# Kernel optimization log

Measured on AMD Instinct MI355X. Metric: run time of the kernel, lower is better.

## Reference

```python
import jax, jax.numpy as jnp
import numpy as np

K = 7          # kernel_size
PAD = K // 2
NAZ, NEL = 12, 5
HID = 64
IC = 2         # input_channels == num_instruments
OC = 2         # output_channels (stereo)
EPS = 1e-5


def conv1d_same(x, w, b):
    # x: (N, Cin, T), w: (Cout, Cin, K) -> (N, Cout, T); cross-correlation like torch
    y = jax.lax.conv_general_dilated(x, w, (1,), 'SAME',
                                     dimension_numbers=('NCH', 'OIH', 'NCH'))
    return y + b[None, :, None]


def batchnorm(x, g, bt):
    # training-mode BatchNorm1d: biased batch stats over (N, T)
    mean = x.mean(axis=(0, 2), keepdims=True)
    var = x.var(axis=(0, 2), keepdims=True)
    return (x - mean) * jax.lax.rsqrt(var + EPS) * g[None, :, None] + bt[None, :, None]


def lrelu(x):
    return jnp.where(x >= 0, x, 0.2 * x)


def setup_inputs() -> dict:
    key = jax.random.key(0)
    ks = jax.random.split(key, 16)
    d = {}
    d['x'] = jax.random.normal(ks[0], (8, IC, 131072), dtype=jnp.float32)
    # spatial_param_net
    d['W1'] = jax.random.normal(ks[1], (HID, IC, K), dtype=jnp.float32) * 0.1
    d['b1'] = jnp.zeros((HID,), jnp.float32)
    d['g1'] = jnp.ones((HID,), jnp.float32)
    d['be1'] = jnp.zeros((HID,), jnp.float32)
    d['W2'] = jax.random.normal(ks[2], (2 * HID, HID, K), dtype=jnp.float32) * 0.05
    d['b2'] = jnp.zeros((2 * HID,), jnp.float32)
    d['g2'] = jnp.ones((2 * HID,), jnp.float32)
    d['be2'] = jnp.zeros((2 * HID,), jnp.float32)
    d['W3'] = jax.random.normal(ks[3], (IC * 3, 2 * HID, K), dtype=jnp.float32) * 0.05
    d['b3'] = jnp.zeros((IC * 3,), jnp.float32)
    # HRTF table: (num_azimuth*num_elevation, output_channels, K)
    d['hrtf'] = jax.random.normal(ks[4], (NAZ * NEL, OC, K), dtype=jnp.float32)
    # binaural_renderer (first conv in-channels = input_channels = 2)
    d['RW1'] = jax.random.normal(ks[5], (HID, IC, K), dtype=jnp.float32) * 0.1
    d['rb1'] = jnp.zeros((HID,), jnp.float32)
    d['rg1'] = jnp.ones((HID,), jnp.float32)
    d['rbe1'] = jnp.zeros((HID,), jnp.float32)
    d['RW2'] = jax.random.normal(ks[6], (2 * HID, HID, K), dtype=jnp.float32) * 0.05
    d['rb2'] = jnp.zeros((2 * HID,), jnp.float32)
    d['rg2'] = jnp.ones((2 * HID,), jnp.float32)
    d['rbe2'] = jnp.zeros((2 * HID,), jnp.float32)
    d['RW3'] = jax.random.normal(ks[7], (OC, 2 * HID, K), dtype=jnp.float32) * 0.05
    d['rb3'] = jnp.zeros((OC,), jnp.float32)
    return d


def reference(x, W1, b1, g1, be1, W2, b2, g2, be2, W3, b3, hrtf,
              RW1, rb1, rg1, rbe1, RW2, rb2, rg2, rbe2, RW3, rb3):
    B, I, T = x.shape
    # spatial parameter network
    h = lrelu(batchnorm(conv1d_same(x, W1, b1), g1, be1))
    h = lrelu(batchnorm(conv1d_same(h, W2, b2), g2, be2))
    sp = jnp.tanh(conv1d_same(h, W3, b3)).reshape(B, I, 3, T)
    # only t=0 of azimuth/elevation/distance is used (matches torch loop)
    az = (sp[:, :, 0, 0] + 1.0) * 0.5 * (NAZ - 1)
    el = (sp[:, :, 1, 0] + 1.0) * 0.5 * (NEL - 1)
    dist = (sp[:, :, 2, 0] + 1.0) * 0.5 * 0.9 + 0.1      # (B, I)
    az_i = jnp.clip(az.astype(jnp.int32), 0, NAZ - 1)
    el_i = jnp.clip(el.astype(jnp.int32), 0, NEL - 1)
    idx = el_i * NAZ + az_i                               # (B, I)
    wg = hrtf[idx]                                        # (B, I, OC, K) gathered filters
    # per-(b,i) conv1d with its gathered HRTF filter, scale by distance, sum over instruments
    xp = jnp.pad(x, ((0, 0), (0, 0), (PAD, PAD)))
    windows = jnp.stack([xp[:, :, k:k + T] for k in range(K)], axis=2)  # (B, I, K, T)
    summed = jnp.einsum('bikt,bick,bi->bct', windows, wg, dist)          # (B, OC, T)
    # binaural renderer
    h = lrelu(batchnorm(conv1d_same(summed, RW1, rb1), rg1, rbe1))
    h = lrelu(batchnorm(conv1d_same(h, RW2, rb2), rg2, rbe2))
    return jnp.tanh(conv1d_same(h, RW3, rb3))
```

## Files before the change

kernel.cpp:

```cpp
#include <hip/hip_runtime.h>
#include <hip/hip_fp16.h>
#include <cstddef>


#define TLEN 131072
#define NB 8
#define NICH 2
#define NHID 64
#define NH2 128
#define EPSV 1e-5f
#define CNTF 1048576.0f
#define FT 120
#define FGRID 1093
#define XCH 1024
#define NCH 128
#define XGRID 1024
#define PREPB 472

typedef _Float16 f16x8 __attribute__((ext_vector_type(8)));
typedef float f32x4 __attribute__((ext_vector_type(4)));

__device__ __forceinline__ float lrelu(float v) { return fmaxf(v, 0.2f * v); }
__device__ __forceinline__ unsigned short h16(float v) {
  return __half_as_ushort(__float2half(v));
}
__device__ __forceinline__ float fh16(unsigned short u) {
  return __half2float(__ushort_as_half(u));
}
__device__ __forceinline__ float ftanh(float x) {
  float e = __expf(2.f * x);
  return 1.f - 2.f / (e + 1.f);
}

__device__ __forceinline__ void prep_body(
    int e,
    const float* __restrict__ W2c, const float* __restrict__ RW2c,
    const float* __restrict__ RW3c,
    const float* __restrict__ W1c, const float* __restrict__ RW1c,
    unsigned short* __restrict__ w2sp, unsigned short* __restrict__ w2re,
    unsigned short* __restrict__ w3g,
    unsigned short* __restrict__ w1sp, unsigned short* __restrict__ w1re)
{
  if (e < 114688) {
    int e2 = (e >= 57344) ? e - 57344 : e;
    int frag = e2 >> 9, within = e2 & 511;
    int c = frag >> 3, mt = frag & 7;
    int mn = within >> 5, kk = within & 31;
    int o = mt * 16 + mn;
    int tap = c >> 1, ch = (c & 1) * 32 + kk;
    const float* src = (e >= 57344) ? RW2c : W2c;
    unsigned short* dst = (e >= 57344) ? w2re : w2sp;
    dst[e2] = h16(src[(o * 64 + ch) * 7 + tap]);
  } else if (e < 116736) {
    int e2 = e - 114688;
    int c = e2 >> 9, within = e2 & 511;
    int m = within >> 5, kk = within & 31;
    int ch = c * 32 + kk;
    w3g[e2] = (m < 14) ? h16(RW3c[((m / 7) * 128 + ch) * 7 + (m % 7)])
                       : (unsigned short)0;
  } else if (e < 120832) {
    int e2 = e - 116736;
    int which = (e2 >= 2048);
    int e3 = e2 & 2047;
    int m = e3 >> 9, w = e3 & 511;
    int mn = w >> 5, K = w & 31;
    int i = K >> 4, kk = K & 15;
    const float* src = which ? RW1c : W1c;
    unsigned short* dst = which ? w1re : w1sp;
    dst[e3] = (kk < 7) ? h16(src[(m * 16 + mn) * 14 + i * 7 + kk])
                       : (unsigned short)0;
  }
}

__device__ __forceinline__ void xcorr_reduce_tail(
    float (&acc)[30], float (*redx)[30], float* __restrict__ partials)
{
  #pragma unroll
  for (int q = 0; q < 30; ++q)
    #pragma unroll
    for (int m = 1; m <= 8; m <<= 1)
      acc[q] += __shfl_xor(acc[q], m, 64);
  const int lane = threadIdx.x & 63, wv = threadIdx.x >> 6;
  if ((lane & 15) == 0) {
    int row = wv * 4 + (lane >> 4);
    #pragma unroll
    for (int q = 0; q < 30; ++q) redx[row][q] = acc[q];
  }
  __syncthreads();
  if (threadIdx.x < 30) {
    float s = 0.f;
    #pragma unroll
    for (int r = 0; r < 16; ++r) s += redx[r][threadIdx.x];
    partials[blockIdx.x * 30 + threadIdx.x] = s;
  }
}

__global__ __launch_bounds__(256) void xcorr_prep(
    const float* __restrict__ z, float* __restrict__ partials,
    const float* __restrict__ W2c, const float* __restrict__ RW2c,
    const float* __restrict__ RW3c,
    const float* __restrict__ W1c, const float* __restrict__ RW1c,
    unsigned short* __restrict__ w2sp, unsigned short* __restrict__ w2re,
    unsigned short* __restrict__ w3g,
    unsigned short* __restrict__ w1sp, unsigned short* __restrict__ w1re)
{
  if (blockIdx.x >= XGRID) {
    int e = (blockIdx.x - XGRID) * 256 + threadIdx.x;
    prep_body(e, W2c, RW2c, RW3c, W1c, RW1c, w2sp, w2re, w3g, w1sp, w1re);
    return;
  }
  const int b = blockIdx.x >> 7;
  const int t0 = (blockIdx.x & (NCH - 1)) * XCH;
  __shared__ float zs[2][XCH + 8];
  __shared__ float redx[16][30];
  #pragma unroll
  for (int i = 0; i < 2; ++i) {
    const float* zp = &z[(size_t)(b * 2 + i) * TLEN + t0];
    *(float4*)&zs[i][threadIdx.x * 4] = *(const float4*)&zp[threadIdx.x * 4];
    if (threadIdx.x < 7) {
      int tg = t0 + XCH + threadIdx.x;
      zs[i][XCH + threadIdx.x] =
          (tg < TLEN) ? z[(size_t)(b * 2 + i) * TLEN + tg] : 0.f;
    }
    if (threadIdx.x == 7) zs[i][XCH + 7] = 0.f;
  }
  __syncthreads();

  float acc[30];
  #pragma unroll
  for (int q = 0; q < 30; ++q) acc[q] = 0.f;
  const int tb = threadIdx.x * 4;
  #pragma unroll
  for (int tt = 0; tt < 4; ++tt) {
    int j = tb + tt;
    float z0 = zs[0][j], z1 = zs[1][j];
    acc[28] += z0; acc[29] += z1;
    #pragma unroll
    for (int d = 0; d < 7; ++d) {
      float a0 = zs[0][j + d], a1 = zs[1][j + d];
      acc[d]      += z0 * a0;
      acc[7 + d]  += z0 * a1;
      acc[14 + d] += z1 * a0;
      acc[21 + d] += z1 * a1;
    }
  }
  xcorr_reduce_tail(acc, redx, partials);
}

__global__ __launch_bounds__(256) void reduce30(
    const float* __restrict__ partials, int nblocks, float* __restrict__ R)
{
  const int q = blockIdx.x;
  float s = 0.f;
  for (int j = threadIdx.x; j < nblocks; j += 256)
    s += partials[j * 30 + q];
  #pragma unroll
  for (int m = 1; m <= 32; m <<= 1) s += __shfl_xor(s, m, 64);
  __shared__ float rs[4];
  if ((threadIdx.x & 63) == 0) rs[threadIdx.x >> 6] = s;
  __syncthreads();
  if (threadIdx.x == 0) R[q] = rs[0] + rs[1] + rs[2] + rs[3];
}

__global__ __launch_bounds__(256) void assemble_coef1(
    const float* __restrict__ Rg,
    const float* __restrict__ W1c, const float* __restrict__ b1c,
    const float* __restrict__ g, const float* __restrict__ be,
    float* __restrict__ coef)
{
  __shared__ float R[30];
  __shared__ float w1s[64 * 14];
  for (int e = threadIdx.x; e < 64 * 14; e += 256) w1s[e] = W1c[e];
  if (threadIdx.x < 30) R[threadIdx.x] = Rg[threadIdx.x];
  __syncthreads();
  if (threadIdx.x < 64) {
    int o = threadIdx.x;
    const float* w = &w1s[o * 14];
    float b1v = b1c[o];
    float sy = 0.f;
    #pragma unroll
    for (int i = 0; i < 2; ++i)
      #pragma unroll
      for (int k = 0; k < 7; ++k) sy += w[i * 7 + k] * R[28 + i];
    float syy = 0.f;
    #pragma unroll
    for (int i = 0; i < 2; ++i)
      #pragma unroll
      for (int k = 0; k < 7; ++k) {
        float wv = w[i * 7 + k];
        #pragma unroll
        for (int i2 = 0; i2 < 2; ++i2)
          #pragma unroll
          for (int k2 = 0; k2 < 7; ++k2) {
            int d = k2 - k;
            float r = (d >= 0) ? R[i * 14 + i2 * 7 + d]
                               : R[i2 * 14 + i * 7 - d];
            syy += wv * w[i2 * 7 + k2] * r;
          }
      }
    float S1 = CNTF * b1v + sy;
    float S2 = 2.f * b1v * S1 - CNTF * b1v * b1v + syy;
    float mean = S1 / CNTF;
    float var = S2 / CNTF - mean * mean;
    float a = g[o] * rsqrtf(var + EPSV);
    coef[o] = a;
    coef[64 + o] = be[o] - mean * a;
  }
}

__global__ __launch_bounds__(256) void reduce_coef(
    const float* __restrict__ partials, int nblocks, int C,
    const float* __restrict__ bso,
    const float* __restrict__ g, const float* __restrict__ be,
    float* __restrict__ coef)
{
  const int c = blockIdx.x;
  float s = 0.f, ss = 0.f;
  for (int j = threadIdx.x; j < nblocks; j += 256) {
    s  += partials[j * 2 * C + c];
    ss += partials[j * 2 * C + C + c];
  }
  #pragma unroll
  for (int off = 32; off >= 1; off >>= 1) {
    s  += __shfl_down(s, off, 64);
    ss += __shfl_down(ss, off, 64);
  }
  __shared__ float rs[4], rss[4];
  const int lane = threadIdx.x & 63, wv = threadIdx.x >> 6;
  if (lane == 0) { rs[wv] = s; rss[wv] = ss; }
  __syncthreads();
  if (threadIdx.x == 0) {
    float st  = rs[0] + rs[1] + rs[2] + rs[3];
    float sst = rss[0] + rss[1] + rss[2] + rss[3];
    float mean = st / CNTF;
    float var  = sst / CNTF - mean * mean;
    float a = g[c] * rsqrtf(var + EPSV);
    float d = be[c] - mean * a;
    coef[c] = a;
    coef[C + c] = d;
    coef[2 * C + c] = d + a * bso[c];
  }
}

__device__ __forceinline__ void stage_x(
    int t0, int xoff, const float* __restrict__ xin, int b, float* xs)
{
  for (int e = threadIdx.x; e < 2 * 168; e += 256) {
    int i = e / 168, j = e % 168;
    int tg = t0 - xoff + j;
    xs[e] = (tg >= 0 && tg < TLEN) ? xin[(b * NICH + i) * TLEN + tg] : 0.f;
  }
}

template<int HOF>
__device__ __forceinline__ void h1_mfma(
    int t0, const float* xs, unsigned short* xw,
    const unsigned short* __restrict__ w1f,
    const float* __restrict__ coef1, const float* __restrict__ b1c,
    unsigned short* h1f)
{
  for (int e = threadIdx.x; e < 144 * 2; e += 256) {
    int n = e >> 1, i = e & 1;
    const float* xp = &xs[i * 168 + n];
    unsigned short hv[7];
    #pragma unroll
    for (int kk = 0; kk < 7; ++kk) hv[kk] = h16(xp[kk]);
    *(uint4*)(xw + n * 32 + i * 16) = make_uint4(
        hv[0] | ((unsigned)hv[1] << 16), hv[2] | ((unsigned)hv[3] << 16),
        hv[4] | ((unsigned)hv[5] << 16), (unsigned)hv[6]);
    *(uint4*)(xw + n * 32 + i * 16 + 8) = make_uint4(0, 0, 0, 0);
  }
  __syncthreads();

  const int lane = threadIdx.x & 63;
  const int wv = threadIdx.x >> 6;
  const int mn = lane & 15, quad = lane >> 4;
  f16x8 A1 = *(const f16x8*)(w1f + wv * 512 + mn * 32 + quad * 8);
  f32x4 acc1[9];
  #pragma unroll
  for (int nt = 0; nt < 9; ++nt) {
    f32x4 z = {0.f, 0.f, 0.f, 0.f};
    acc1[nt] = z;
  }
  #pragma unroll
  for (int nt = 0; nt < 9; ++nt) {
    f16x8 bb = *(const f16x8*)(xw + (nt * 16 + mn) * 32 + quad * 8);
    acc1[nt] = __builtin_amdgcn_mfma_f32_16x16x32_f16(A1, bb, acc1[nt], 0, 0, 0);
  }
  const int ch0 = wv * 16 + quad * 4;
  float a1v[4], dd[4];
  #pragma unroll
  for (int r = 0; r < 4; ++r) {
    a1v[r] = coef1[ch0 + r];
    dd[r]  = coef1[64 + ch0 + r] + a1v[r] * b1c[ch0 + r];
  }
  #pragma unroll
  for (int nt = 0; nt < 9; ++nt) {
    int n = nt * 16 + mn;
    int t = t0 - HOF + n;
    bool ok = (t >= 0) && (t < TLEN);
    unsigned us[4];
    #pragma unroll
    for (int r = 0; r < 4; ++r) {
      float v = lrelu(a1v[r] * acc1[nt][r] + dd[r]);
      us[r] = h16(ok ? v : 0.f);
    }
    *(uint2*)(h1f + n * 72 + ch0) =
        make_uint2(us[0] | (us[1] << 16), us[2] | (us[3] << 16));
  }
}

template<int SAVE>
__global__ __launch_bounds__(256, 4) void conv2_stats_mfma(
    const float* __restrict__ xin,
    const unsigned short* __restrict__ w1f, const float* __restrict__ b1c,
    const float* __restrict__ coef1,
    const unsigned short* __restrict__ w2f,
    const float* __restrict__ b2c,
    float* __restrict__ partials,
    unsigned short* __restrict__ h1out)
{
  const int b  = blockIdx.x >> 10;
  const int t0 = (blockIdx.x & 1023) * 128;

  __shared__ __align__(16) char smem[31296];
  unsigned short* h1f = (unsigned short*)smem;
  float* xs = (float*)(smem + 20736);
  unsigned short* xw = (unsigned short*)(smem + 22080);
  float* redS = (float*)smem;
  float* redSS= (float*)(smem + 8704);

  stage_x(t0, 6, xin, b, xs);
  __syncthreads();
  h1_mfma<3>(t0, xs, xw, w1f, coef1, b1c, h1f);
  __syncthreads();

  if (SAVE == 1) {
    for (int e = threadIdx.x; e < 1024; e += 256) {
      int row = e >> 3, c8 = (e & 7) * 8;
      *(uint4*)(h1out + ((size_t)(b * TLEN + t0 + row) * 64 + c8)) =
          *(const uint4*)(h1f + (row + 3) * 72 + c8);
    }
  }

  const int lane = threadIdx.x & 63;
  const int wv = threadIdx.x >> 6;
  const int mn = lane & 15, quad = lane >> 4;

  f32x4 acc[2][8];
  #pragma unroll
  for (int mt = 0; mt < 2; ++mt)
    #pragma unroll
    for (int nt = 0; nt < 8; ++nt) {
      f32x4 z = {0.f, 0.f, 0.f, 0.f};
      acc[mt][nt] = z;
    }

  f16x8 ca[2], na[2];
  auto loadA = [&](int c, f16x8 (&A)[2]) {
    #pragma unroll
    for (int mt = 0; mt < 2; ++mt)
      A[mt] = *(const f16x8*)(w2f + (c * 8 + wv * 2 + mt) * 512 + mn * 32 + quad * 8);
  };
  loadA(0, ca);
  #pragma unroll
  for (int c = 0; c < 14; ++c) {
    if (c < 13) loadA(c + 1, na);
    const int tap = c >> 1;
    const int ch0 = (c & 1) * 32 + quad * 8;
    #pragma unroll
    for (int nt = 0; nt < 8; ++nt) {
      f16x8 bb = *(const f16x8*)(h1f + (nt * 16 + mn + tap) * 72 + ch0);
      acc[0][nt] = __builtin_amdgcn_mfma_f32_16x16x32_f16(ca[0], bb, acc[0][nt], 0, 0, 0);
      acc[1][nt] = __builtin_amdgcn_mfma_f32_16x16x32_f16(ca[1], bb, acc[1][nt], 0, 0, 0);
    }
    ca[0] = na[0]; ca[1] = na[1];
  }
  __syncthreads();

  #pragma unroll
  for (int mt = 0; mt < 2; ++mt)
    #pragma unroll
    for (int r = 0; r < 4; ++r) {
      int o = (wv * 2 + mt) * 16 + quad * 4 + r;
      float bo = b2c[o];
      float s = 0.f, ss = 0.f;
      #pragma unroll
      for (int nt = 0; nt < 8; ++nt) {
        float v = acc[mt][nt][r] + bo;
        s += v; ss += v * v;
      }
      redS[o * 17 + mn] = s;
      redSS[o * 17 + mn] = ss;
    }
  __syncthreads();
  {
    int o = threadIdx.x & 127;
    const float* src = (threadIdx.x < 128) ? redS : redSS;
    float s = 0.f;
    #pragma unroll
    for (int j = 0; j < 16; ++j) s += src[o * 17 + j];
    partials[blockIdx.x * 256 + threadIdx.x] = s;
  }
}

__global__ __launch_bounds__(256) void finalize_spatial(
    const float* __restrict__ x,
    const float* __restrict__ W1c, const float* __restrict__ b1c,
    const float* __restrict__ coef1,
    const float* __restrict__ W2c, const float* __restrict__ b2c,
    const float* __restrict__ coef2,
    const float* __restrict__ W3c, const float* __restrict__ b3c,
    const float* __restrict__ hrtf, float* __restrict__ wgbuf)
{
  const int bb = blockIdx.x;
  __shared__ float xl[2 * 16];
  __shared__ float h1l[64 * 10];
  __shared__ float h2l[NH2 * 4];
  __shared__ float sp[6];
  const int tid = threadIdx.x;
  if (tid < 32) {
    int i = tid >> 4, j = tid & 15;
    int t = j - 6;
    xl[tid] = (t >= 0) ? x[(bb * 2 + i) * TLEN + t] : 0.f;
  }
  __syncthreads();
  if (tid < 64) {
    int ch = tid;
    float a1 = coef1[ch], d1 = coef1[64 + ch], bo = b1c[ch];
    for (int tt = 0; tt < 10; ++tt) {
      float acc = bo;
      #pragma unroll
      for (int i2 = 0; i2 < 2; ++i2)
        #pragma unroll
        for (int k = 0; k < 7; ++k)
          acc += xl[i2 * 16 + tt + k] * W1c[ch * 14 + i2 * 7 + k];
      float v = lrelu(a1 * acc + d1);
      h1l[ch * 10 + tt] = (tt >= 3) ? v : 0.f;
    }
  }
  __syncthreads();
  if (tid < NH2) {
    int o = tid;
    float a2 = coef2[o], d2 = coef2[NH2 + o], bo = b2c[o];
    float acc[4] = {bo, bo, bo, bo};
    for (int i = 0; i < 64; ++i)
      #pragma unroll
      for (int k = 0; k < 7; ++k) {
        float w = W2c[(o * 64 + i) * 7 + k];
        #pragma unroll
        for (int t = 0; t < 4; ++t)
          acc[t] += h1l[i * 10 + t + k] * w;
      }
    #pragma unroll
    for (int t = 0; t < 4; ++t)
      h2l[o * 4 + t] = lrelu(a2 * acc[t] + d2);
  }
  __syncthreads();
  if (tid < 6) {
    int c3 = tid;
    float acc = b3c[c3];
    for (int c = 0; c < NH2; ++c)
      #pragma unroll
      for (int k = 3; k < 7; ++k)
        acc += h2l[c * 4 + (k - 3)] * W3c[(c3 * NH2 + c) * 7 + k];
    sp[c3] = tanhf(acc);
  }
  __syncthreads();
  if (tid < 2) {
    int i = tid;
    float az = (sp[i * 3 + 0] + 1.f) * 0.5f * 11.f;
    float el = (sp[i * 3 + 1] + 1.f) * 0.5f * 4.f;
    float dist = (sp[i * 3 + 2] + 1.f) * 0.5f * 0.9f + 0.1f;
    int azi = min(max((int)az, 0), 11);
    int eli = min(max((int)el, 0), 4);
    int idx = eli * 12 + azi;
    for (int e = 0; e < 14; ++e)
      wgbuf[(bb * 2 + i) * 14 + e] = hrtf[idx * 14 + e] * dist;
  }
}

__global__ __launch_bounds__(256) void mix_xcorr(
    const float* __restrict__ x, const float* __restrict__ wgbuf,
    float* __restrict__ summed, float* __restrict__ partials)
{
  const int b = blockIdx.x >> 7;
  const int t0 = (blockIdx.x & (NCH - 1)) * XCH;
  const int tid = threadIdx.x;
  __shared__ float xs2[2][XCH + 20];
  __shared__ float zs[2][XCH + 8];
  __shared__ float redx[16][30];

  float wv[2][2][7];
  #pragma unroll
  for (int i = 0; i < 2; ++i)
    #pragma unroll
    for (int c = 0; c < 2; ++c)
      #pragma unroll
      for (int k = 0; k < 7; ++k)
        wv[i][c][k] = wgbuf[(b * 2 + i) * 14 + c * 7 + k];

  const bool interior = (t0 >= 8) && (t0 + XCH + 12 <= TLEN);
  if (interior) {
    #pragma unroll
    for (int i = 0; i < 2; ++i) {
      const float* xp = &x[(size_t)(b * 2 + i) * TLEN + t0 - 8];
      *(float4*)&xs2[i][tid * 4] = *(const float4*)&xp[tid * 4];
      if (tid < 5)
        *(float4*)&xs2[i][XCH + tid * 4] = *(const float4*)&xp[XCH + tid * 4];
    }
  } else {
    for (int e = tid; e < 2 * (XCH + 20); e += 256) {
      int i = e / (XCH + 20), j = e % (XCH + 20);
      int tg = t0 - 8 + j;
      xs2[i][j] = (tg >= 0 && tg < TLEN) ? x[(size_t)(b * 2 + i) * TLEN + tg]
                                         : 0.f;
    }
  }
  __syncthreads();

  const int tb = tid * 4;
  {
    float xl[2][10];
    #pragma unroll
    for (int i = 0; i < 2; ++i)
      #pragma unroll
      for (int j = 0; j < 10; ++j) xl[i][j] = xs2[i][tb + 5 + j];
    float acc[2][4] = {{0.f, 0.f, 0.f, 0.f}, {0.f, 0.f, 0.f, 0.f}};
    #pragma unroll
    for (int i = 0; i < 2; ++i)
      #pragma unroll
      for (int c = 0; c < 2; ++c)
        #pragma unroll
        for (int k = 0; k < 7; ++k)
          #pragma unroll
          for (int tt = 0; tt < 4; ++tt)
            acc[c][tt] += xl[i][tt + k] * wv[i][c][k];
    #pragma unroll
    for (int c = 0; c < 2; ++c) {
      *(float4*)&zs[c][tb] =
          make_float4(acc[c][0], acc[c][1], acc[c][2], acc[c][3]);
      *reinterpret_cast<float4*>(&summed[(size_t)(b * 2 + c) * TLEN + t0 + tb]) =
          make_float4(acc[c][0], acc[c][1], acc[c][2], acc[c][3]);
    }
  }
  if (tid < 7) {
    int t = t0 + XCH + tid;
    float s0 = 0.f, s1 = 0.f;
    if (t < TLEN) {
      #pragma unroll
      for (int i = 0; i < 2; ++i)
        #pragma unroll
        for (int k = 0; k < 7; ++k) {
          float xv = xs2[i][XCH + tid + 5 + k];
          s0 += xv * wv[i][0][k];
          s1 += xv * wv[i][1][k];
        }
    }
    zs[0][XCH + tid] = s0;
    zs[1][XCH + tid] = s1;
  }
  if (tid == 7) { zs[0][XCH + 7] = 0.f; zs[1][XCH + 7] = 0.f; }
  __syncthreads();

  float acc[30];
  #pragma unroll
  for (int q = 0; q < 30; ++q) acc[q] = 0.f;
  #pragma unroll
  for (int tt = 0; tt < 4; ++tt) {
    int j = tb + tt;
    float z0 = zs[0][j], z1 = zs[1][j];
    acc[28] += z0; acc[29] += z1;
    #pragma unroll
    for (int d = 0; d < 7; ++d) {
      float a0 = zs[0][j + d], a1 = zs[1][j + d];
      acc[d]      += z0 * a0;
      acc[7 + d]  += z0 * a1;
      acc[14 + d] += z1 * a0;
      acc[21 + d] += z1 * a1;
    }
  }
  xcorr_reduce_tail(acc, redx, partials);
}

__device__ __forceinline__ void final_tail(
    int b, int t0, f32x4 (&acc)[2][8],
    const float* __restrict__ coef2,
    const unsigned short* __restrict__ w3g, const float* __restrict__ rb3c,
    unsigned short* h2t, unsigned short* dq, float* __restrict__ out)
{
  const int lane = threadIdx.x & 63;
  const int wv = threadIdx.x >> 6;
  const int mn = lane & 15, quad = lane >> 4;

  float a2v[2][4], dd2[2][4];
  #pragma unroll
  for (int mt = 0; mt < 2; ++mt)
    #pragma unroll
    for (int r = 0; r < 4; ++r) {
      int o = (wv * 2 + mt) * 16 + quad * 4 + r;
      a2v[mt][r] = coef2[o];
      dd2[mt][r] = coef2[2 * NH2 + o];
    }
  __syncthreads();

  #pragma unroll
  for (int nt = 0; nt < 8; ++nt) {
    int jp = nt * 16 + mn;
    int t = t0 - 3 + jp;
    bool ok = (t >= 0) && (t < TLEN);
    #pragma unroll
    for (int mt = 0; mt < 2; ++mt) {
      int obase = (wv * 2 + mt) * 16 + quad * 4;
      unsigned us[4];
      #pragma unroll
      for (int r = 0; r < 4; ++r) {
        float v = lrelu(a2v[mt][r] * acc[mt][nt][r] + dd2[mt][r]);
        us[r] = h16(ok ? v : 0.f);
      }
      *(uint2*)(h2t + jp * 136 + obase) =
          make_uint2(us[0] | (us[1] << 16), us[2] | (us[3] << 16));
    }
  }
  __syncthreads();

  const int nt0 = wv * 2;
  f32x4 acc3[2];
  #pragma unroll
  for (int i = 0; i < 2; ++i) {
    f32x4 z = {0.f, 0.f, 0.f, 0.f};
    acc3[i] = z;
  }
  #pragma unroll
  for (int c = 0; c < 4; ++c) {
    f16x8 A3 = *(const f16x8*)(w3g + c * 512 + mn * 32 + quad * 8);
    #pragma unroll
    for (int i = 0; i < 2; ++i) {
      f16x8 bb = *(const f16x8*)(h2t + ((nt0 + i) * 16 + mn) * 136 + c * 32 + quad * 8);
      acc3[i] = __builtin_amdgcn_mfma_f32_16x16x32_f16(A3, bb, acc3[i], 0, 0, 0);
    }
  }
  #pragma unroll
  for (int i = 0; i < 2; ++i) {
    int n = (nt0 + i) * 16 + mn;
    unsigned us[4];
    #pragma unroll
    for (int r = 0; r < 4; ++r) us[r] = h16(acc3[i][r]);
    *(uint2*)(dq + n * 20 + quad * 4) =
        make_uint2(us[0] | (us[1] << 16), us[2] | (us[3] << 16));
  }
  __syncthreads();

  {
    int tid = threadIdx.x;
    if (tid < 240) {
      int oc = (tid >= FT) ? 1 : 0;
      int u = tid - oc * FT;
      float s = rb3c[oc];
      #pragma unroll
      for (int tap = 0; tap < 7; ++tap)
        s += fh16(dq[(u + tap) * 20 + oc * 7 + tap]);
      int t = t0 + u;
      if (t < TLEN) out[(b * 2 + oc) * TLEN + t] = ftanh(s);
    }
  }
}

__device__ __forceinline__ void conv2_loop(
    const unsigned short* h1f, const unsigned short* __restrict__ w2f,
    f32x4 (&acc)[2][8])
{
  const int lane = threadIdx.x & 63;
  const int wv = threadIdx.x >> 6;
  const int mn = lane & 15, quad = lane >> 4;
  #pragma unroll
  for (int mt = 0; mt < 2; ++mt)
    #pragma unroll
    for (int nt = 0; nt < 8; ++nt) {
      f32x4 z = {0.f, 0.f, 0.f, 0.f};
      acc[mt][nt] = z;
    }
  f16x8 ca[2], na[2];
  auto loadA = [&](int c, f16x8 (&A)[2]) {
    #pragma unroll
    for (int mt = 0; mt < 2; ++mt)
      A[mt] = *(const f16x8*)(w2f + (c * 8 + wv * 2 + mt) * 512 + mn * 32 + quad * 8);
  };
  loadA(0, ca);
  #pragma unroll
  for (int c = 0; c < 14; ++c) {
    if (c < 13) loadA(c + 1, na);
    const int tap = c >> 1;
    const int ch0 = (c & 1) * 32 + quad * 8;
    #pragma unroll
    for (int nt = 0; nt < 8; ++nt) {
      f16x8 bb = *(const f16x8*)(h1f + (nt * 16 + mn + tap) * 72 + ch0);
      acc[0][nt] = __builtin_amdgcn_mfma_f32_16x16x32_f16(ca[0], bb, acc[0][nt], 0, 0, 0);
      acc[1][nt] = __builtin_amdgcn_mfma_f32_16x16x32_f16(ca[1], bb, acc[1][nt], 0, 0, 0);
    }
    ca[0] = na[0]; ca[1] = na[1];
  }
}

__global__ __launch_bounds__(256, 4) void conv2_final_mfma(
    const float* __restrict__ xin,
    const unsigned short* __restrict__ w1f, const float* __restrict__ b1c,
    const float* __restrict__ coef1,
    const unsigned short* __restrict__ w2f,
    const float* __restrict__ coef2,
    const unsigned short* __restrict__ w3g, const float* __restrict__ rb3c,
    float* __restrict__ out)
{
  const int b  = blockIdx.y;
  const int t0 = blockIdx.x * FT;

  __shared__ __align__(16) char smem[39936];
  unsigned short* h1f = (unsigned short*)smem;
  float* xs = (float*)(smem + 20736);
  unsigned short* xw = (unsigned short*)(smem + 22080);
  unsigned short* h2t = (unsigned short*)smem;
  unsigned short* dq  = (unsigned short*)(smem + 34816);

  stage_x(t0, 9, xin, b, xs);
  __syncthreads();
  h1_mfma<6>(t0, xs, xw, w1f, coef1, b1c, h1f);
  __syncthreads();

  f32x4 acc[2][8];
  conv2_loop(h1f, w2f, acc);
  final_tail(b, t0, acc, coef2, w3g, rb3c, h2t, dq, out);
}

__global__ __launch_bounds__(256, 4) void conv2_final_h1(
    const unsigned short* __restrict__ h1g,
    const unsigned short* __restrict__ w2f,
    const float* __restrict__ coef2,
    const unsigned short* __restrict__ w3g, const float* __restrict__ rb3c,
    float* __restrict__ out)
{
  const int b  = blockIdx.y;
  const int t0 = blockIdx.x * FT;

  __shared__ __align__(16) char smem[39936];
  unsigned short* h1f = (unsigned short*)smem;
  unsigned short* h2t = (unsigned short*)smem;
  unsigned short* dq  = (unsigned short*)(smem + 34816);

  for (int e = threadIdx.x; e < 144 * 8; e += 256) {
    int r = e >> 3, c8 = (e & 7) * 8;
    int t = t0 - 6 + r;
    uint4 v = make_uint4(0, 0, 0, 0);
    if (t >= 0 && t < TLEN)
      v = *(const uint4*)(h1g + ((size_t)(b * TLEN + t) * 64 + c8));
    *(uint4*)(h1f + r * 72 + c8) = v;
  }
  __syncthreads();

  f32x4 acc[2][8];
  conv2_loop(h1f, w2f, acc);
  final_tail(b, t0, acc, coef2, w3g, rb3c, h2t, dq, out);
}

extern "C" void kernel_launch(void* const* d_in, const int* in_sizes, int n_in,
                              void* d_out, int out_size, void* d_ws, size_t ws_size,
                              hipStream_t stream)
{
  (void)in_sizes; (void)n_in; (void)out_size;
  const float* x    = (const float*)d_in[0];
  const float* W1   = (const float*)d_in[1];
  const float* b1   = (const float*)d_in[2];
  const float* g1   = (const float*)d_in[3];
  const float* be1  = (const float*)d_in[4];
  const float* W2   = (const float*)d_in[5];
  const float* b2   = (const float*)d_in[6];
  const float* g2   = (const float*)d_in[7];
  const float* be2  = (const float*)d_in[8];
  const float* W3   = (const float*)d_in[9];
  const float* b3   = (const float*)d_in[10];
  const float* hrtf = (const float*)d_in[11];
  const float* RW1  = (const float*)d_in[12];
  const float* rb1  = (const float*)d_in[13];
  const float* rg1  = (const float*)d_in[14];
  const float* rbe1 = (const float*)d_in[15];
  const float* RW2  = (const float*)d_in[16];
  const float* rb2  = (const float*)d_in[17];
  const float* rg2  = (const float*)d_in[18];
  const float* rbe2 = (const float*)d_in[19];
  const float* RW3  = (const float*)d_in[20];
  const float* rb3  = (const float*)d_in[21];
  float* out = (float*)d_out;

  float* partialsB = (float*)d_out;

  char* ws = (char*)d_ws;
  float* partialsA      = (float*)(ws + 0);
  float* summed         = (float*)(ws + 524288);
  float* coef1          = (float*)(ws + 8912896);
  float* coef2          = (float*)(ws + 8913408);
  float* coefR1         = (float*)(ws + 8914944);
  float* coefR2         = (float*)(ws + 8915456);
  float* wgbuf          = (float*)(ws + 8916992);
  unsigned short* w2sp  = (unsigned short*)(ws + 8918016);
  unsigned short* w2re  = (unsigned short*)(ws + 9032704);
  unsigned short* w3g   = (unsigned short*)(ws + 9147392);
  unsigned short* w1sp  = (unsigned short*)(ws + 9151488);
  unsigned short* w1re  = (unsigned short*)(ws + 9155584);
  float* Rbuf           = (float*)(ws + 9159680);
  unsigned short* h1g   = (unsigned short*)(ws + 16777216);
  const size_t WS_NEEDED_MID = 16777216ull + 134217728ull;
  const bool mid = ws_size >= WS_NEEDED_MID;

  xcorr_prep<<<XGRID + PREPB, 256, 0, stream>>>(
      x, partialsA, W2, RW2, RW3, W1, RW1, w2sp, w2re, w3g, w1sp, w1re);
  reduce30<<<30, 256, 0, stream>>>(partialsA, XGRID, Rbuf);
  assemble_coef1<<<1, 256, 0, stream>>>(Rbuf, W1, b1, g1, be1, coef1);
  conv2_stats_mfma<0><<<8192, 256, 0, stream>>>(x, w1sp, b1, coef1, w2sp,
                                                b2, partialsB, nullptr);
  reduce_coef<<<128, 256, 0, stream>>>(partialsB, 8192, 128, b2, g2, be2, coef2);
  finalize_spatial<<<8, 256, 0, stream>>>(x, W1, b1, coef1, W2, b2, coef2,
                                          W3, b3, hrtf, wgbuf);
  mix_xcorr<<<XGRID, 256, 0, stream>>>(x, wgbuf, summed, partialsA);
  reduce30<<<30, 256, 0, stream>>>(partialsA, XGRID, Rbuf);
  assemble_coef1<<<1, 256, 0, stream>>>(Rbuf, RW1, rb1, rg1, rbe1, coefR1);
  if (mid) {
    conv2_stats_mfma<1><<<8192, 256, 0, stream>>>(summed, w1re, rb1, coefR1,
                                                  w2re, rb2, partialsB, h1g);
  } else {
    conv2_stats_mfma<0><<<8192, 256, 0, stream>>>(summed, w1re, rb1, coefR1,
                                                  w2re, rb2, partialsB, nullptr);
  }
  reduce_coef<<<128, 256, 0, stream>>>(partialsB, 8192, 128, rb2, rg2, rbe2, coefR2);
  if (mid) {
    conv2_final_h1<<<dim3(FGRID, NB), 256, 0, stream>>>(
        h1g, w2re, coefR2, w3g, rb3, out);
  } else {
    conv2_final_mfma<<<dim3(FGRID, NB), 256, 0, stream>>>(
        summed, w1re, rb1, coefR1, w2re, coefR2, w3g, rb3, out);
  }
}
```

Measured before the change: 571.0 us.

## Cache pre-norm conv2 output for renderer batches and fuse stat reduction

For as many batches as the workspace allows, the renderer's conv2 stats pass now writes the raw conv2 output as fp16 instead of h1. A new lightweight final kernel then applies BN and leaky ReLU, followed by the small conv3, with no second conv2 MFMA pass. The remaining batches keep the existing h1-reload path. The reduce30 and assemble_coef1 kernels are merged into one single-block kernel to cut launches. The trade is extra HBM traffic and workspace per cached batch, plus fp16 rounding of pre-norm activations.

```diff
diff --git a/kernel.cpp b/kernel.cpp
--- a/kernel.cpp
+++ b/kernel.cpp
@@ -147,31 +147,29 @@
   xcorr_reduce_tail(acc, redx, partials);
 }
 
-__global__ __launch_bounds__(256) void reduce30(
-    const float* __restrict__ partials, int nblocks, float* __restrict__ R)
-{
-  const int q = blockIdx.x;
-  float s = 0.f;
-  for (int j = threadIdx.x; j < nblocks; j += 256)
-    s += partials[j * 30 + q];
-  #pragma unroll
-  for (int m = 1; m <= 32; m <<= 1) s += __shfl_xor(s, m, 64);
-  __shared__ float rs[4];
-  if ((threadIdx.x & 63) == 0) rs[threadIdx.x >> 6] = s;
-  __syncthreads();
-  if (threadIdx.x == 0) R[q] = rs[0] + rs[1] + rs[2] + rs[3];
-}
-
-__global__ __launch_bounds__(256) void assemble_coef1(
-    const float* __restrict__ Rg,
+__global__ __launch_bounds__(256) void reduce_assemble(
+    const float* __restrict__ partials, int nblocks,
     const float* __restrict__ W1c, const float* __restrict__ b1c,
     const float* __restrict__ g, const float* __restrict__ be,
     float* __restrict__ coef)
 {
+  __shared__ float pr[8][30];
   __shared__ float R[30];
   __shared__ float w1s[64 * 14];
   for (int e = threadIdx.x; e < 64 * 14; e += 256) w1s[e] = W1c[e];
-  if (threadIdx.x < 30) R[threadIdx.x] = Rg[threadIdx.x];
+  if (threadIdx.x < 240) {
+    int q = threadIdx.x % 30, chunk = threadIdx.x / 30;
+    float s = 0.f;
+    for (int j = chunk; j < nblocks; j += 8) s += partials[j * 30 + q];
+    pr[chunk][q] = s;
+  }
+  __syncthreads();
+  if (threadIdx.x < 30) {
+    float s = 0.f;
+    #pragma unroll
+    for (int c = 0; c < 8; ++c) s += pr[c][threadIdx.x];
+    R[threadIdx.x] = s;
+  }
   __syncthreads();
   if (threadIdx.x < 64) {
     int o = threadIdx.x;
@@ -318,7 +316,8 @@
     const unsigned short* __restrict__ w2f,
     const float* __restrict__ b2c,
     float* __restrict__ partials,
-    unsigned short* __restrict__ h1out)
+    unsigned short* __restrict__ h1out,
+    unsigned short* __restrict__ h2out, int nb2)
 {
   const int b  = blockIdx.x >> 10;
   const int t0 = (blockIdx.x & 1023) * 128;
@@ -335,10 +334,10 @@
   h1_mfma<3>(t0, xs, xw, w1f, coef1, b1c, h1f);
   __syncthreads();
 
-  if (SAVE == 1) {
+  if (SAVE == 1 && b >= nb2) {
     for (int e = threadIdx.x; e < 1024; e += 256) {
       int row = e >> 3, c8 = (e & 7) * 8;
-      *(uint4*)(h1out + ((size_t)(b * TLEN + t0 + row) * 64 + c8)) =
+      *(uint4*)(h1out + ((size_t)((b - nb2) * TLEN + t0 + row) * 64 + c8)) =
           *(const uint4*)(h1f + (row + 3) * 72 + c8);
     }
   }
@@ -375,6 +374,23 @@
       acc[1][nt] = __builtin_amdgcn_mfma_f32_16x16x32_f16(ca[1], bb, acc[1][nt], 0, 0, 0);
     }
     ca[0] = na[0]; ca[1] = na[1];
+  }
+
+  if (SAVE == 1 && b < nb2) {
+    #pragma unroll
+    for (int mt = 0; mt < 2; ++mt) {
+      int o0 = (wv * 2 + mt) * 16 + quad * 4;
+      #pragma unroll
+      for (int nt = 0; nt < 8; ++nt) {
+        int jp = nt * 16 + mn;
+        unsigned lo = (unsigned)h16(acc[mt][nt][0]) |
+                      ((unsigned)h16(acc[mt][nt][1]) << 16);
+        unsigned hi = (unsigned)h16(acc[mt][nt][2]) |
+                      ((unsigned)h16(acc[mt][nt][3]) << 16);
+        *(uint2*)(h2out + ((size_t)(b * TLEN) + t0 + jp) * 128 + o0) =
+            make_uint2(lo, hi);
+      }
+    }
   }
   __syncthreads();
 
@@ -732,13 +748,14 @@
 }
 
 __global__ __launch_bounds__(256, 4) void conv2_final_h1(
-    const unsigned short* __restrict__ h1g,
+    const unsigned short* __restrict__ h1g, int bbase,
     const unsigned short* __restrict__ w2f,
     const float* __restrict__ coef2,
     const unsigned short* __restrict__ w3g, const float* __restrict__ rb3c,
     float* __restrict__ out)
 {
-  const int b  = blockIdx.y;
+  const int bslot = blockIdx.y;
+  const int b  = bbase + bslot;
   const int t0 = blockIdx.x * FT;
 
   __shared__ __align__(16) char smem[39936];
@@ -751,7 +768,7 @@
     int t = t0 - 6 + r;
     uint4 v = make_uint4(0, 0, 0, 0);
     if (t >= 0 && t < TLEN)
-      v = *(const uint4*)(h1g + ((size_t)(b * TLEN + t) * 64 + c8));
+      v = *(const uint4*)(h1g + ((size_t)(bslot * TLEN + t) * 64 + c8));
     *(uint4*)(h1f + r * 72 + c8) = v;
   }
   __syncthreads();
@@ -759,6 +776,94 @@
   f32x4 acc[2][8];
   conv2_loop(h1f, w2f, acc);
   final_tail(b, t0, acc, coef2, w3g, rb3c, h2t, dq, out);
+}
+
+__global__ __launch_bounds__(256, 4) void render_final_light(
+    const unsigned short* __restrict__ h2s,
+    const float* __restrict__ coef2,
+    const unsigned short* __restrict__ w3g, const float* __restrict__ rb3c,
+    float* __restrict__ out)
+{
+  const int b  = blockIdx.y;
+  const int t0 = blockIdx.x * FT;
+
+  __shared__ __align__(16) char smem[39936];
+  unsigned short* h2t = (unsigned short*)smem;
+  unsigned short* dq  = (unsigned short*)(smem + 34816);
+
+  const int c8 = (threadIdx.x & 15) * 8;
+  float a2r[8], d2r[8];
+  #pragma unroll
+  for (int j = 0; j < 8; ++j) {
+    a2r[j] = coef2[c8 + j];
+    d2r[j] = coef2[2 * NH2 + c8 + j];
+  }
+  for (int e = threadIdx.x; e < 2048; e += 256) {
+    int row = e >> 4;
+    int t = t0 - 3 + row;
+    uint4 pk = make_uint4(0, 0, 0, 0);
+    if (t >= 0 && t < TLEN) {
+      uint4 rv = *(const uint4*)(h2s + ((size_t)(b * TLEN + t) * 128 + c8));
+      unsigned w[4] = {rv.x, rv.y, rv.z, rv.w};
+      unsigned ow[4];
+      #pragma unroll
+      for (int j = 0; j < 4; ++j) {
+        float vlo = lrelu(a2r[2 * j] * fh16((unsigned short)(w[j] & 0xffff)) +
+                          d2r[2 * j]);
+        float vhi = lrelu(a2r[2 * j + 1] * fh16((unsigned short)(w[j] >> 16)) +
+                          d2r[2 * j + 1]);
+        ow[j] = (unsigned)h16(vlo) | ((unsigned)h16(vhi) << 16);
+      }
+      pk = make_uint4(ow[0], ow[1], ow[2], ow[3]);
+    }
+    *(uint4*)(h2t + row * 136 + c8) = pk;
+  }
+  __syncthreads();
+
+  const int lane = threadIdx.x & 63;
+  const int wv = threadIdx.x >> 6;
+  const int mn = lane & 15, quad = lane >> 4;
+
+  const int nt0 = wv * 2;
+  f32x4 acc3[2];
+  #pragma unroll
+  for (int i = 0; i < 2; ++i) {
+    f32x4 z = {0.f, 0.f, 0.f, 0.f};
+    acc3[i] = z;
+  }
+  #pragma unroll
+  for (int c = 0; c < 4; ++c) {
+    f16x8 A3 = *(const f16x8*)(w3g + c * 512 + mn * 32 + quad * 8);
+    #pragma unroll
+    for (int i = 0; i < 2; ++i) {
+      f16x8 bb = *(const f16x8*)(h2t + ((nt0 + i) * 16 + mn) * 136 + c * 32 + quad * 8);
+      acc3[i] = __builtin_amdgcn_mfma_f32_16x16x32_f16(A3, bb, acc3[i], 0, 0, 0);
+    }
+  }
+  #pragma unroll
+  for (int i = 0; i < 2; ++i) {
+    int n = (nt0 + i) * 16 + mn;
+    unsigned us[4];
+    #pragma unroll
+    for (int r = 0; r < 4; ++r) us[r] = h16(acc3[i][r]);
+    *(uint2*)(dq + n * 20 + quad * 4) =
+        make_uint2(us[0] | (us[1] << 16), us[2] | (us[3] << 16));
+  }
+  __syncthreads();
+
+  {
+    int tid = threadIdx.x;
+    if (tid < 240) {
+      int oc = (tid >= FT) ? 1 : 0;
+      int u = tid - oc * FT;
+      float s = rb3c[oc];
+      #pragma unroll
+      for (int tap = 0; tap < 7; ++tap)
+        s += fh16(dq[(u + tap) * 20 + oc * 7 + tap]);
+      int t = t0 + u;
+      if (t < TLEN) out[(b * 2 + oc) * TLEN + t] = ftanh(s);
+    }
+  }
 }
 
 extern "C" void kernel_launch(void* const* d_in, const int* in_sizes, int n_in,
@@ -805,34 +910,51 @@
   unsigned short* w3g   = (unsigned short*)(ws + 9147392);
   unsigned short* w1sp  = (unsigned short*)(ws + 9151488);
   unsigned short* w1re  = (unsigned short*)(ws + 9155584);
-  float* Rbuf           = (float*)(ws + 9159680);
-  unsigned short* h1g   = (unsigned short*)(ws + 16777216);
-  const size_t WS_NEEDED_MID = 16777216ull + 134217728ull;
-  const bool mid = ws_size >= WS_NEEDED_MID;
+
+  const size_t BASE  = 16777216ull;
+  const size_t PERH1 = 16777216ull;
+  const size_t PERH2 = 33554432ull;
+  const bool mid = ws_size >= BASE + 8 * PERH1;
+  int nb2 = 0;
+  if (mid) {
+    long long extra = (long long)ws_size - (long long)(BASE + 8 * PERH1);
+    nb2 = (int)(extra / (long long)PERH1);
+    if (nb2 > 8) nb2 = 8;
+    if (nb2 < 0) nb2 = 0;
+  }
+  unsigned short* h2g = (unsigned short*)(ws + BASE);
+  unsigned short* h1g = (unsigned short*)(ws + BASE + (size_t)nb2 * PERH2);
 
   xcorr_prep<<<XGRID + PREPB, 256, 0, stream>>>(
       x, partialsA, W2, RW2, RW3, W1, RW1, w2sp, w2re, w3g, w1sp, w1re);
-  reduce30<<<30, 256, 0, stream>>>(partialsA, XGRID, Rbuf);
-  assemble_coef1<<<1, 256, 0, stream>>>(Rbuf, W1, b1, g1, be1, coef1);
+  reduce_assemble<<<1, 256, 0, stream>>>(partialsA, XGRID, W1, b1, g1, be1,
+                                         coef1);
   conv2_stats_mfma<0><<<8192, 256, 0, stream>>>(x, w1sp, b1, coef1, w2sp,
-                                                b2, partialsB, nullptr);
+                                                b2, partialsB, nullptr,
+                                                nullptr, 0);
   reduce_coef<<<128, 256, 0, stream>>>(partialsB, 8192, 128, b2, g2, be2, coef2);
   finalize_spatial<<<8, 256, 0, stream>>>(x, W1, b1, coef1, W2, b2, coef2,
                                           W3, b3, hrtf, wgbuf);
   mix_xcorr<<<XGRID, 256, 0, stream>>>(x, wgbuf, summed, partialsA);
-  reduce30<<<30, 256, 0, stream>>>(partialsA, XGRID, Rbuf);
-  assemble_coef1<<<1, 256, 0, stream>>>(Rbuf, RW1, rb1, rg1, rbe1, coefR1);
+  reduce_assemble<<<1, 256, 0, stream>>>(partialsA, XGRID, RW1, rb1, rg1,
+                                         rbe1, coefR1);
   if (mid) {
     conv2_stats_mfma<1><<<8192, 256, 0, stream>>>(summed, w1re, rb1, coefR1,
-                                                  w2re, rb2, partialsB, h1g);
+                                                  w2re, rb2, partialsB,
+                                                  h1g, h2g, nb2);
   } else {
     conv2_stats_mfma<0><<<8192, 256, 0, stream>>>(summed, w1re, rb1, coefR1,
-                                                  w2re, rb2, partialsB, nullptr);
+                                                  w2re, rb2, partialsB,
+                                                  nullptr, nullptr, 0);
   }
   reduce_coef<<<128, 256, 0, stream>>>(partialsB, 8192, 128, rb2, rg2, rbe2, coefR2);
   if (mid) {
-    conv2_final_h1<<<dim3(FGRID, NB), 256, 0, stream>>>(
-        h1g, w2re, coefR2, w3g, rb3, out);
+    if (nb2 > 0)
+      render_final_light<<<dim3(FGRID, nb2), 256, 0, stream>>>(
+          h2g, coefR2, w3g, rb3, out);
+    if (nb2 < 8)
+      conv2_final_h1<<<dim3(FGRID, 8 - nb2), 256, 0, stream>>>(
+          h1g, nb2, w2re, coefR2, w3g, rb3, out);
   } else {
     conv2_final_mfma<<<dim3(FGRID, NB), 256, 0, stream>>>(
         summed, w1re, rb1, coefR1, w2re, coefR2, w3g, rb3, out);
```

New measurement: 622.8 us. 9.1% more time.
